# Optimization experiments

Measured on AMD Instinct MI355X. Metric: run time of the kernel, lower is better.

Reference implementation:

```python
import jax, jax.numpy as jnp
import numpy as np

B, S, HID = 2, 2048, 2048
H, KVH, D = 16, 4, 128
GROUPS = H // KVH  # 4


def apply_rotary(x, cos, sin):
    # x: [B, h, S, D]; cos/sin: [S, D//2]
    xr = x[..., 0::2]
    xi = x[..., 1::2]
    c = cos[None, None, :, :]
    s = sin[None, None, :, :]
    orr = xr * c - xi * s
    oi = xr * s + xi * c
    return jnp.stack([orr, oi], axis=-1).reshape(x.shape)


def setup_inputs() -> dict:
    key = jax.random.key(0)
    k0, k1, k2, k3, k4 = jax.random.split(key, 5)
    x = jax.random.normal(k0, (B, S, HID), dtype=jnp.float32)
    # real RoPE frequencies (llama-style), stored as [S, D//2, 2] = (cos, sin)
    inv_freq = 1.0 / (10000.0 ** (np.arange(0, D, 2, dtype=np.float32) / D))
    t = np.arange(S, dtype=np.float32)
    ang = np.outer(t, inv_freq)  # [S, D//2]
    freqs_cis = jnp.asarray(np.stack([np.cos(ang), np.sin(ang)], axis=-1), dtype=jnp.float32)
    sc = 0.02
    wq = jax.random.normal(k1, (HID, H * D), dtype=jnp.float32) * sc
    wk = jax.random.normal(k2, (HID, KVH * D), dtype=jnp.float32) * sc
    wv = jax.random.normal(k3, (HID, KVH * D), dtype=jnp.float32) * sc
    wo = jax.random.normal(k4, (H * D, HID), dtype=jnp.float32) * sc
    return {"x": x, "freqs_cis": freqs_cis, "wq": wq, "wk": wk, "wv": wv, "wo": wo}


def reference(x, freqs_cis, wq, wk, wv, wo):
    b, s, _ = x.shape
    cos, sin = freqs_cis[..., 0], freqs_cis[..., 1]
    q = (x @ wq).reshape(b, s, H, D).transpose(0, 2, 1, 3)    # [B,H,S,D]
    k = (x @ wk).reshape(b, s, KVH, D).transpose(0, 2, 1, 3)  # [B,KVH,S,D]
    v = (x @ wv).reshape(b, s, KVH, D).transpose(0, 2, 1, 3)
    q = apply_rotary(q, cos, sin)
    k = apply_rotary(k, cos, sin)
    # GQA expand: repeat kv heads into query-head groups
    k = jnp.repeat(k, GROUPS, axis=1)  # [B,H,S,D]
    v = jnp.repeat(v, GROUPS, axis=1)
    scale = 1.0 / jnp.sqrt(jnp.asarray(D, dtype=x.dtype))
    scores = jnp.einsum("bhqd,bhkd->bhqk", q, k) * scale
    causal = jnp.tril(jnp.ones((s, s), dtype=bool))
    scores = jnp.where(causal[None, None], scores, jnp.asarray(-jnp.inf, dtype=scores.dtype))
    attn = jax.nn.softmax(scores, axis=-1)
    out = jnp.einsum("bhqk,bhkd->bhqd", attn, v)
    out = out.transpose(0, 2, 1, 3).reshape(b, s, H * D)
    return out @ wo
```

## Files before the change

### kernel.cpp

```cpp
#include <hip/hip_runtime.h>
#include <hip/hip_bf16.h>

#define B_   2
#define S_   2048
#define HID_ 2048
#define H_   16
#define KVH_ 4
#define D_   128
#define M_   4096
#define NQKV 3072

typedef __attribute__((ext_vector_type(8))) short bf16x8;
typedef __attribute__((ext_vector_type(4))) float f32x4;
typedef const __attribute__((address_space(1))) unsigned int* gas_p;
typedef __attribute__((address_space(3))) unsigned int* las_p;

__device__ __forceinline__ unsigned short f2b(float f) {
    __hip_bfloat16 h = __float2bfloat16(f);
    return *reinterpret_cast<unsigned short*>(&h);
}
__device__ __forceinline__ float b2f(unsigned short u) {
    __hip_bfloat16 h;
    *reinterpret_cast<unsigned short*>(&h) = u;
    return __bfloat162float(h);
}

__global__ __launch_bounds__(256)
void convert_x(const float* __restrict__ x, unsigned short* __restrict__ xb) {
    int i = (blockIdx.x * 256 + threadIdx.x) * 4;
    float4 v = *(const float4*)(x + i);
    ushort4 o;
    o.x = f2b(v.x); o.y = f2b(v.y); o.z = f2b(v.z); o.w = f2b(v.w);
    *(ushort4*)(xb + i) = o;
}

__global__ __launch_bounds__(256)
void convert_w_t(const float* __restrict__ w, int N,
                 unsigned short* __restrict__ wt, int nbase) {
    __shared__ float tile[32][33];
    int tx = threadIdx.x & 31, ty = threadIdx.x >> 5;
    int n0 = blockIdx.x * 32, k0 = blockIdx.y * 32;
    #pragma unroll
    for (int j = 0; j < 4; j++)
        tile[ty + j*8][tx] = w[(size_t)(k0 + ty + j*8) * N + n0 + tx];
    __syncthreads();
    #pragma unroll
    for (int j = 0; j < 4; j++)
        wt[(size_t)(nbase + n0 + ty + j*8) * 2048 + k0 + tx] = f2b(tile[tx][ty + j*8]);
}

template<bool BF16OUT>
__global__ __launch_bounds__(256)
void gemm_bt(const unsigned short* __restrict__ A,
             const unsigned short* __restrict__ BT,
             void* __restrict__ Cv, int N) {
    __shared__ unsigned short As[128][32];
    __shared__ unsigned short Bs[128][32];

    int tid  = threadIdx.x;
    int lane = tid & 63, w = tid >> 6;
    int quad = lane >> 4, l15 = lane & 15;
    int row0 = blockIdx.y * 128, col0 = blockIdx.x * 128;
    int wm = (w & 1) * 64, wn = (w >> 1) * 64;

    f32x4 acc[4][4];
    const f32x4 zf = {0.f, 0.f, 0.f, 0.f};
    #pragma unroll
    for (int i = 0; i < 4; i++)
        #pragma unroll
        for (int j = 0; j < 4; j++) acc[i][j] = zf;

    const unsigned short* Arow = A  + (size_t)row0 * 2048;
    const unsigned short* Brow = BT + (size_t)col0 * 2048;

    for (int k0 = 0; k0 < 2048; k0 += 32) {
        #pragma unroll
        for (int it = 0; it < 2; it++) {
            int c = w * 128 + it * 64 + lane;
            int r = c >> 2, q8 = (c & 3) * 8;
            __builtin_amdgcn_global_load_lds(
                (gas_p)(Arow + (size_t)r * 2048 + k0 + q8),
                (las_p)((char*)&As[0][0] + (size_t)(w * 128 + it * 64) * 16),
                16, 0, 0);
            __builtin_amdgcn_global_load_lds(
                (gas_p)(Brow + (size_t)r * 2048 + k0 + q8),
                (las_p)((char*)&Bs[0][0] + (size_t)(w * 128 + it * 64) * 16),
                16, 0, 0);
        }
        __syncthreads();
        bf16x8 af[4], bf[4];
        #pragma unroll
        for (int i = 0; i < 4; i++) af[i] = *(const bf16x8*)&As[wm + i*16 + l15][quad * 8];
        #pragma unroll
        for (int j = 0; j < 4; j++) bf[j] = *(const bf16x8*)&Bs[wn + j*16 + l15][quad * 8];
        #pragma unroll
        for (int i = 0; i < 4; i++)
            #pragma unroll
            for (int j = 0; j < 4; j++)
                acc[i][j] = __builtin_amdgcn_mfma_f32_16x16x32_bf16(af[i], bf[j], acc[i][j], 0, 0, 0);
        __syncthreads();
    }

    #pragma unroll
    for (int i = 0; i < 4; i++)
        #pragma unroll
        for (int j = 0; j < 4; j++)
            #pragma unroll
            for (int r = 0; r < 4; r++) {
                size_t idx = (size_t)(row0 + wm + i*16 + quad*4 + r) * N + col0 + wn + j*16 + l15;
                if (BF16OUT) ((unsigned short*)Cv)[idx] = f2b(acc[i][j][r]);
                else         ((float*)Cv)[idx] = acc[i][j][r];
            }
}

__global__ __launch_bounds__(256)
void rope_kernel(unsigned short* __restrict__ qkv, const float* __restrict__ freqs) {
    int p = blockIdx.x * 256 + threadIdx.x;
    int m = p / 1280;
    int cp = p - m * 1280;
    int col = cp * 2;
    int s = m & (S_ - 1);
    int d = col & (D_ - 1);
    unsigned short* ptr = qkv + (size_t)m * NQKV + col;
    ushort2 uv = *(ushort2*)ptr;
    float xr = b2f(uv.x), xi = b2f(uv.y);
    float cs = freqs[s * 128 + d], sn = freqs[s * 128 + d + 1];
    ushort2 ov;
    ov.x = f2b(xr * cs - xi * sn);
    ov.y = f2b(xr * sn + xi * cs);
    *(ushort2*)ptr = ov;
}

__global__ __launch_bounds__(256)
void v_transpose(const unsigned short* __restrict__ qkv, unsigned short* __restrict__ vT) {
    __shared__ unsigned short tile[32][34];
    int tx = threadIdx.x & 31, ty = threadIdx.x >> 5;
    int s0 = blockIdx.x * 32;
    int c0 = blockIdx.y * 32;
    int b  = blockIdx.z;
    #pragma unroll
    for (int j = 0; j < 4; j++)
        tile[ty + j*8][tx] = qkv[(size_t)(b*2048 + s0 + ty + j*8) * NQKV + 2560 + c0 + tx];
    __syncthreads();
    #pragma unroll
    for (int j = 0; j < 4; j++)
        vT[(size_t)(b*512 + c0 + ty + j*8) * 2048 + s0 + tx] = tile[tx][ty + j*8];
}

__global__ __launch_bounds__(256)
void attn_mfma(const unsigned short* __restrict__ qkv,
               const unsigned short* __restrict__ vT,
               unsigned short* __restrict__ ao) {
    __shared__ unsigned short Ks[64 * 128];
    __shared__ unsigned short Vt[128 * 64];

    int tid  = threadIdx.x;
    int lane = tid & 63, w = tid >> 6;
    int quad = lane >> 4, l15 = lane & 15;
    int qt = 31 - blockIdx.x;
    int h = blockIdx.y, b = blockIdx.z;
    int hk = h >> 2;
    int q0 = qt * 64;
    const float scale = 0.08838834764831845f;

    bf16x8 aq[4];
    {
        const unsigned short* qrow = qkv + (size_t)(b*2048 + q0 + w*16 + l15) * NQKV + h*128;
        #pragma unroll
        for (int k4 = 0; k4 < 4; k4++)
            aq[k4] = *(const bf16x8*)(qrow + k4*32 + quad*8);
    }

    int koff[4][4];
    #pragma unroll
    for (int j = 0; j < 4; j++) {
        int row = ((j >> 1) * 32) + ((l15 >> 2) * 8) + ((j & 1) * 4) + (l15 & 3);
        #pragma unroll
        for (int k4 = 0; k4 < 4; k4++) {
            int slot = (k4 * 4 + quad) ^ (row & 15);
            koff[j][k4] = (row * 16 + slot) * 8;
        }
    }
    int voff[8][2];
    #pragma unroll
    for (int jn = 0; jn < 8; jn++) {
        int row = jn * 16 + l15;
        #pragma unroll
        for (int sh = 0; sh < 2; sh++) {
            int slot = (sh * 4 + quad) ^ (row & 7);
            voff[jn][sh] = (row * 8 + slot) * 8;
        }
    }

    const unsigned short* kb0 = qkv + (size_t)(b*2048) * NQKV + 2048 + hk*128;
    const unsigned short* vb0 = vT + (size_t)(b*512 + hk*128) * 2048;

    auto stage_k = [&](int kt) {
        #pragma unroll
        for (int it = 0; it < 4; it++) {
            int s = w * 256 + it * 64 + lane;
            int r = s >> 4, qp = s & 15;
            int q = qp ^ (r & 15);
            __builtin_amdgcn_global_load_lds(
                (gas_p)(kb0 + (size_t)(kt*64 + r) * NQKV + q * 8),
                (las_p)((char*)&Ks[0] + (w * 256 + it * 64) * 16),
                16, 0, 0);
        }
    };
    auto stage_v = [&](int kt) {
        #pragma unroll
        for (int it = 0; it < 4; it++) {
            int s = w * 256 + it * 64 + lane;
            int r = s >> 3, qp = s & 7;
            int q = qp ^ (r & 7);
            __builtin_amdgcn_global_load_lds(
                (gas_p)(vb0 + (size_t)r * 2048 + kt*64 + q * 8),
                (las_p)((char*)&Vt[0] + (w * 256 + it * 64) * 16),
                16, 0, 0);
        }
    };

    f32x4 o_acc[8];
    const f32x4 zf = {0.f, 0.f, 0.f, 0.f};
    #pragma unroll
    for (int jn = 0; jn < 8; jn++) o_acc[jn] = zf;
    float m_i = -1e30f, l_i = 0.f;
    const int qglob = q0 + w*16 + l15;

    stage_k(0);
    for (int kt = 0; kt <= qt; kt++) {
        __syncthreads();
        stage_v(kt);

        f32x4 s_acc[4];
        #pragma unroll
        for (int j = 0; j < 4; j++) {
            s_acc[j] = zf;
            #pragma unroll
            for (int k4 = 0; k4 < 4; k4++) {
                bf16x8 ak = *(const bf16x8*)&Ks[koff[j][k4]];
                s_acc[j] = __builtin_amdgcn_mfma_f32_16x16x32_bf16(ak, aq[k4], s_acc[j], 0, 0, 0);
            }
        }

        float sv[4][4];
        #pragma unroll
        for (int j = 0; j < 4; j++)
            #pragma unroll
            for (int r = 0; r < 4; r++)
                sv[j][r] = s_acc[j][r] * scale;
        if (kt == qt) {
            #pragma unroll
            for (int j = 0; j < 4; j++)
                #pragma unroll
                for (int r = 0; r < 4; r++) {
                    int sloc = ((j >> 1) * 32) + quad*8 + ((j & 1) * 4) + r;
                    if (kt*64 + sloc > qglob) sv[j][r] = -1e30f;
                }
        }

        float mx = sv[0][0];
        #pragma unroll
        for (int j = 0; j < 4; j++)
            #pragma unroll
            for (int r = 0; r < 4; r++) mx = fmaxf(mx, sv[j][r]);
        mx = fmaxf(mx, __shfl_xor(mx, 16));
        mx = fmaxf(mx, __shfl_xor(mx, 32));
        float mnew = fmaxf(m_i, mx);
        float alpha = __expf(m_i - mnew);
        float p[4][4], rs = 0.f;
        #pragma unroll
        for (int j = 0; j < 4; j++)
            #pragma unroll
            for (int r = 0; r < 4; r++) {
                p[j][r] = __expf(sv[j][r] - mnew);
                rs += p[j][r];
            }
        l_i = l_i * alpha + rs;
        m_i = mnew;
        #pragma unroll
        for (int jn = 0; jn < 8; jn++)
            #pragma unroll
            for (int r = 0; r < 4; r++) o_acc[jn][r] *= alpha;

        bf16x8 pp0, pp1;
        #pragma unroll
        for (int r = 0; r < 4; r++) {
            pp0[r]     = (short)f2b(p[0][r]);
            pp0[r + 4] = (short)f2b(p[1][r]);
            pp1[r]     = (short)f2b(p[2][r]);
            pp1[r + 4] = (short)f2b(p[3][r]);
        }

        __syncthreads();
        if (kt < qt) stage_k(kt + 1);

        #pragma unroll
        for (int jn = 0; jn < 8; jn++) {
            bf16x8 av0 = *(const bf16x8*)&Vt[voff[jn][0]];
            bf16x8 av1 = *(const bf16x8*)&Vt[voff[jn][1]];
            o_acc[jn] = __builtin_amdgcn_mfma_f32_16x16x32_bf16(av0, pp0, o_acc[jn], 0, 0, 0);
            o_acc[jn] = __builtin_amdgcn_mfma_f32_16x16x32_bf16(av1, pp1, o_acc[jn], 0, 0, 0);
        }
    }

    float lt = l_i;
    lt += __shfl_xor(lt, 16);
    lt += __shfl_xor(lt, 32);
    float inv = 1.f / lt;

    size_t base = (size_t)(b*2048 + qglob) * 2048 + h*128;
    #pragma unroll
    for (int jn = 0; jn < 8; jn++) {
        ushort4 ov;
        ov.x = f2b(o_acc[jn][0] * inv);
        ov.y = f2b(o_acc[jn][1] * inv);
        ov.z = f2b(o_acc[jn][2] * inv);
        ov.w = f2b(o_acc[jn][3] * inv);
        *(ushort4*)(ao + base + jn*16 + quad*4) = ov;
    }
}

extern "C" void kernel_launch(void* const* d_in, const int* in_sizes, int n_in,
                              void* d_out, int out_size, void* d_ws, size_t ws_size,
                              hipStream_t stream) {
    const float* x     = (const float*)d_in[0];
    const float* freqs = (const float*)d_in[1];
    const float* wq    = (const float*)d_in[2];
    const float* wk    = (const float*)d_in[3];
    const float* wv    = (const float*)d_in[4];
    const float* wo    = (const float*)d_in[5];
    float* out = (float*)d_out;

    char* ws = (char*)d_ws;
    unsigned short* xbf    = (unsigned short*)(ws);
    unsigned short* aobuf  = (unsigned short*)(ws);
    unsigned short* wqkvT  = (unsigned short*)(ws + (16u<<20));
    unsigned short* woT    = (unsigned short*)(ws + (28u<<20));
    unsigned short* qkvbuf = (unsigned short*)(ws + (36u<<20));
    unsigned short* vTbuf  = (unsigned short*)(ws + (60u<<20));

    dim3 blk(256);
    convert_x<<<8192, blk, 0, stream>>>(x, xbf);
    convert_w_t<<<dim3(64, 64), blk, 0, stream>>>(wq, 2048, wqkvT, 0);
    convert_w_t<<<dim3(16, 64), blk, 0, stream>>>(wk,  512, wqkvT, 2048);
    convert_w_t<<<dim3(16, 64), blk, 0, stream>>>(wv,  512, wqkvT, 2560);
    convert_w_t<<<dim3(64, 64), blk, 0, stream>>>(wo, 2048, woT, 0);

    gemm_bt<true><<<dim3(NQKV/128, M_/128), blk, 0, stream>>>(xbf, wqkvT, qkvbuf, NQKV);
    rope_kernel<<<20480, blk, 0, stream>>>(qkvbuf, freqs);
    v_transpose<<<dim3(64, 16, 2), blk, 0, stream>>>(qkvbuf, vTbuf);
    attn_mfma<<<dim3(32, 16, 2), blk, 0, stream>>>(qkvbuf, vTbuf, aobuf);
    gemm_bt<false><<<dim3(2048/128, M_/128), blk, 0, stream>>>(aobuf, woT, out, 2048);
}
```

Before: 355.8 us.

## Split long causal query tiles across two blocks and merge partial softmax results

The attention kernel now runs with 128 threads per block, and each wave handles two 16-row query fragments so that every K fragment read from LDS feeds two MFMAs. Query tiles in the upper half of the causal range have their KV loop split across two blocks. One half writes an unnormalised-merge partial output plus (max, sum) statistics into workspace, and a new merge kernel rescales and combines the two halves into the output. The aim is to balance the triangular causal workload and shorten the tail, at the cost of an extra launch, workspace traffic and a bf16 round-trip on the partial outputs.

```diff
diff --git a/kernel.cpp b/kernel.cpp
--- a/kernel.cpp
+++ b/kernel.cpp
@@ -147,28 +147,43 @@
         vT[(size_t)(b*512 + c0 + ty + j*8) * 2048 + s0 + tx] = tile[tx][ty + j*8];
 }
 
-__global__ __launch_bounds__(256)
+__global__ __launch_bounds__(128)
 void attn_mfma(const unsigned short* __restrict__ qkv,
                const unsigned short* __restrict__ vT,
-               unsigned short* __restrict__ ao) {
+               unsigned short* __restrict__ ao,
+               unsigned short* __restrict__ wsP,
+               float2* __restrict__ wsML) {
     __shared__ unsigned short Ks[64 * 128];
     __shared__ unsigned short Vt[128 * 64];
 
     int tid  = threadIdx.x;
     int lane = tid & 63, w = tid >> 6;
     int quad = lane >> 4, l15 = lane & 15;
-    int qt = 31 - blockIdx.x;
-    int h = blockIdx.y, b = blockIdx.z;
+    int bx = blockIdx.x, h = blockIdx.y, b = blockIdx.z;
     int hk = h >> 2;
+
+    int qt, c;
+    bool split = (bx < 32);
+    if (split) { qt = 31 - (bx >> 1); c = bx & 1; }
+    else       { qt = 47 - bx;        c = 0;      }
+    int nt = qt + 1;
+    int kt_begin = 0, kt_end = nt;
+    if (split) {
+        int nt0 = (nt + 1) >> 1;
+        kt_begin = c ? nt0 : 0;
+        kt_end   = c ? nt  : nt0;
+    }
     int q0 = qt * 64;
     const float scale = 0.08838834764831845f;
 
-    bf16x8 aq[4];
-    {
-        const unsigned short* qrow = qkv + (size_t)(b*2048 + q0 + w*16 + l15) * NQKV + h*128;
+    bf16x8 aq[2][4];
+    #pragma unroll
+    for (int qf = 0; qf < 2; qf++) {
+        const unsigned short* qrow =
+            qkv + (size_t)(b*2048 + q0 + w*32 + qf*16 + l15) * NQKV + h*128;
         #pragma unroll
         for (int k4 = 0; k4 < 4; k4++)
-            aq[k4] = *(const bf16x8*)(qrow + k4*32 + quad*8);
+            aq[qf][k4] = *(const bf16x8*)(qrow + k4*32 + quad*8);
     }
 
     int koff[4][4];
@@ -181,144 +196,190 @@
             koff[j][k4] = (row * 16 + slot) * 8;
         }
     }
-    int voff[8][2];
-    #pragma unroll
-    for (int jn = 0; jn < 8; jn++) {
-        int row = jn * 16 + l15;
-        #pragma unroll
-        for (int sh = 0; sh < 2; sh++) {
-            int slot = (sh * 4 + quad) ^ (row & 7);
-            voff[jn][sh] = (row * 8 + slot) * 8;
-        }
-    }
+    int vbase0 = (l15 * 8 + (quad ^ (l15 & 7))) * 8;
+    int vbase1 = (l15 * 8 + ((4 + quad) ^ (l15 & 7))) * 8;
 
     const unsigned short* kb0 = qkv + (size_t)(b*2048) * NQKV + 2048 + hk*128;
     const unsigned short* vb0 = vT + (size_t)(b*512 + hk*128) * 2048;
 
     auto stage_k = [&](int kt) {
         #pragma unroll
-        for (int it = 0; it < 4; it++) {
-            int s = w * 256 + it * 64 + lane;
+        for (int it = 0; it < 8; it++) {
+            int s = w * 512 + it * 64 + lane;
             int r = s >> 4, qp = s & 15;
             int q = qp ^ (r & 15);
             __builtin_amdgcn_global_load_lds(
                 (gas_p)(kb0 + (size_t)(kt*64 + r) * NQKV + q * 8),
-                (las_p)((char*)&Ks[0] + (w * 256 + it * 64) * 16),
+                (las_p)((char*)&Ks[0] + (w * 512 + it * 64) * 16),
                 16, 0, 0);
         }
     };
     auto stage_v = [&](int kt) {
         #pragma unroll
-        for (int it = 0; it < 4; it++) {
-            int s = w * 256 + it * 64 + lane;
+        for (int it = 0; it < 8; it++) {
+            int s = w * 512 + it * 64 + lane;
             int r = s >> 3, qp = s & 7;
             int q = qp ^ (r & 7);
             __builtin_amdgcn_global_load_lds(
                 (gas_p)(vb0 + (size_t)r * 2048 + kt*64 + q * 8),
-                (las_p)((char*)&Vt[0] + (w * 256 + it * 64) * 16),
+                (las_p)((char*)&Vt[0] + (w * 512 + it * 64) * 16),
                 16, 0, 0);
         }
     };
 
-    f32x4 o_acc[8];
+    f32x4 o_acc[2][8];
     const f32x4 zf = {0.f, 0.f, 0.f, 0.f};
     #pragma unroll
-    for (int jn = 0; jn < 8; jn++) o_acc[jn] = zf;
-    float m_i = -1e30f, l_i = 0.f;
-    const int qglob = q0 + w*16 + l15;
-
-    stage_k(0);
-    for (int kt = 0; kt <= qt; kt++) {
+    for (int qf = 0; qf < 2; qf++)
+        #pragma unroll
+        for (int jn = 0; jn < 8; jn++) o_acc[qf][jn] = zf;
+    float m_i[2] = {-1e30f, -1e30f}, l_i[2] = {0.f, 0.f};
+    int qglob[2] = {q0 + w*32 + l15, q0 + w*32 + 16 + l15};
+
+    stage_k(kt_begin);
+    for (int kt = kt_begin; kt < kt_end; kt++) {
         __syncthreads();
         stage_v(kt);
 
-        f32x4 s_acc[4];
+        f32x4 s_acc[2][4];
         #pragma unroll
         for (int j = 0; j < 4; j++) {
-            s_acc[j] = zf;
+            s_acc[0][j] = zf; s_acc[1][j] = zf;
             #pragma unroll
             for (int k4 = 0; k4 < 4; k4++) {
                 bf16x8 ak = *(const bf16x8*)&Ks[koff[j][k4]];
-                s_acc[j] = __builtin_amdgcn_mfma_f32_16x16x32_bf16(ak, aq[k4], s_acc[j], 0, 0, 0);
+                s_acc[0][j] = __builtin_amdgcn_mfma_f32_16x16x32_bf16(ak, aq[0][k4], s_acc[0][j], 0, 0, 0);
+                s_acc[1][j] = __builtin_amdgcn_mfma_f32_16x16x32_bf16(ak, aq[1][k4], s_acc[1][j], 0, 0, 0);
             }
         }
 
-        float sv[4][4];
-        #pragma unroll
-        for (int j = 0; j < 4; j++)
-            #pragma unroll
-            for (int r = 0; r < 4; r++)
-                sv[j][r] = s_acc[j][r] * scale;
-        if (kt == qt) {
+        bf16x8 pp[2][2];
+        #pragma unroll
+        for (int qf = 0; qf < 2; qf++) {
+            float sv[4][4];
+            #pragma unroll
+            for (int j = 0; j < 4; j++)
+                #pragma unroll
+                for (int r = 0; r < 4; r++)
+                    sv[j][r] = s_acc[qf][j][r] * scale;
+            if (kt == qt) {
+                #pragma unroll
+                for (int j = 0; j < 4; j++)
+                    #pragma unroll
+                    for (int r = 0; r < 4; r++) {
+                        int sloc = ((j >> 1) * 32) + quad*8 + ((j & 1) * 4) + r;
+                        if (kt*64 + sloc > qglob[qf]) sv[j][r] = -1e30f;
+                    }
+            }
+            float mx = sv[0][0];
+            #pragma unroll
+            for (int j = 0; j < 4; j++)
+                #pragma unroll
+                for (int r = 0; r < 4; r++) mx = fmaxf(mx, sv[j][r]);
+            mx = fmaxf(mx, __shfl_xor(mx, 16));
+            mx = fmaxf(mx, __shfl_xor(mx, 32));
+            float mnew = fmaxf(m_i[qf], mx);
+            float alpha = __expf(m_i[qf] - mnew);
+            float rs = 0.f;
+            float p[4][4];
             #pragma unroll
             for (int j = 0; j < 4; j++)
                 #pragma unroll
                 for (int r = 0; r < 4; r++) {
-                    int sloc = ((j >> 1) * 32) + quad*8 + ((j & 1) * 4) + r;
-                    if (kt*64 + sloc > qglob) sv[j][r] = -1e30f;
+                    p[j][r] = __expf(sv[j][r] - mnew);
+                    rs += p[j][r];
                 }
-        }
-
-        float mx = sv[0][0];
-        #pragma unroll
-        for (int j = 0; j < 4; j++)
-            #pragma unroll
-            for (int r = 0; r < 4; r++) mx = fmaxf(mx, sv[j][r]);
-        mx = fmaxf(mx, __shfl_xor(mx, 16));
-        mx = fmaxf(mx, __shfl_xor(mx, 32));
-        float mnew = fmaxf(m_i, mx);
-        float alpha = __expf(m_i - mnew);
-        float p[4][4], rs = 0.f;
-        #pragma unroll
-        for (int j = 0; j < 4; j++)
+            l_i[qf] = l_i[qf] * alpha + rs;
+            m_i[qf] = mnew;
+            #pragma unroll
+            for (int jn = 0; jn < 8; jn++)
+                #pragma unroll
+                for (int r = 0; r < 4; r++) o_acc[qf][jn][r] *= alpha;
             #pragma unroll
             for (int r = 0; r < 4; r++) {
-                p[j][r] = __expf(sv[j][r] - mnew);
-                rs += p[j][r];
+                pp[qf][0][r]     = (short)f2b(p[0][r]);
+                pp[qf][0][r + 4] = (short)f2b(p[1][r]);
+                pp[qf][1][r]     = (short)f2b(p[2][r]);
+                pp[qf][1][r + 4] = (short)f2b(p[3][r]);
             }
-        l_i = l_i * alpha + rs;
-        m_i = mnew;
-        #pragma unroll
-        for (int jn = 0; jn < 8; jn++)
-            #pragma unroll
-            for (int r = 0; r < 4; r++) o_acc[jn][r] *= alpha;
-
-        bf16x8 pp0, pp1;
-        #pragma unroll
-        for (int r = 0; r < 4; r++) {
-            pp0[r]     = (short)f2b(p[0][r]);
-            pp0[r + 4] = (short)f2b(p[1][r]);
-            pp1[r]     = (short)f2b(p[2][r]);
-            pp1[r + 4] = (short)f2b(p[3][r]);
         }
 
         __syncthreads();
-        if (kt < qt) stage_k(kt + 1);
+        if (kt + 1 < kt_end) stage_k(kt + 1);
 
         #pragma unroll
         for (int jn = 0; jn < 8; jn++) {
-            bf16x8 av0 = *(const bf16x8*)&Vt[voff[jn][0]];
-            bf16x8 av1 = *(const bf16x8*)&Vt[voff[jn][1]];
-            o_acc[jn] = __builtin_amdgcn_mfma_f32_16x16x32_bf16(av0, pp0, o_acc[jn], 0, 0, 0);
-            o_acc[jn] = __builtin_amdgcn_mfma_f32_16x16x32_bf16(av1, pp1, o_acc[jn], 0, 0, 0);
-        }
-    }
-
-    float lt = l_i;
-    lt += __shfl_xor(lt, 16);
-    lt += __shfl_xor(lt, 32);
-    float inv = 1.f / lt;
-
-    size_t base = (size_t)(b*2048 + qglob) * 2048 + h*128;
-    #pragma unroll
-    for (int jn = 0; jn < 8; jn++) {
-        ushort4 ov;
-        ov.x = f2b(o_acc[jn][0] * inv);
-        ov.y = f2b(o_acc[jn][1] * inv);
-        ov.z = f2b(o_acc[jn][2] * inv);
-        ov.w = f2b(o_acc[jn][3] * inv);
-        *(ushort4*)(ao + base + jn*16 + quad*4) = ov;
-    }
+            bf16x8 av0 = *(const bf16x8*)&Vt[jn*1024 + vbase0];
+            bf16x8 av1 = *(const bf16x8*)&Vt[jn*1024 + vbase1];
+            o_acc[0][jn] = __builtin_amdgcn_mfma_f32_16x16x32_bf16(av0, pp[0][0], o_acc[0][jn], 0, 0, 0);
+            o_acc[0][jn] = __builtin_amdgcn_mfma_f32_16x16x32_bf16(av1, pp[0][1], o_acc[0][jn], 0, 0, 0);
+            o_acc[1][jn] = __builtin_amdgcn_mfma_f32_16x16x32_bf16(av0, pp[1][0], o_acc[1][jn], 0, 0, 0);
+            o_acc[1][jn] = __builtin_amdgcn_mfma_f32_16x16x32_bf16(av1, pp[1][1], o_acc[1][jn], 0, 0, 0);
+        }
+    }
+
+    int pidx = ((qt - 16) * 16 + h) * 2 + b;
+    #pragma unroll
+    for (int qf = 0; qf < 2; qf++) {
+        float lt = l_i[qf];
+        lt += __shfl_xor(lt, 16);
+        lt += __shfl_xor(lt, 32);
+        float inv = 1.f / lt;
+        int q_local = w*32 + qf*16 + l15;
+        unsigned short* dst;
+        if (!split || c == 1)
+            dst = ao + (size_t)(b*2048 + q0 + q_local) * 2048 + h*128;
+        else
+            dst = wsP + (size_t)pidx * 8192 + q_local * 128;
+        #pragma unroll
+        for (int jn = 0; jn < 8; jn++) {
+            ushort4 ov;
+            ov.x = f2b(o_acc[qf][jn][0] * inv);
+            ov.y = f2b(o_acc[qf][jn][1] * inv);
+            ov.z = f2b(o_acc[qf][jn][2] * inv);
+            ov.w = f2b(o_acc[qf][jn][3] * inv);
+            *(ushort4*)(dst + jn*16 + quad*4) = ov;
+        }
+        if (split && quad == 0)
+            wsML[(pidx*2 + c) * 64 + q_local] = make_float2(m_i[qf], lt);
+    }
+}
+
+__global__ __launch_bounds__(256)
+void merge_kernel(unsigned short* __restrict__ ao,
+                  const unsigned short* __restrict__ wsP,
+                  const float2* __restrict__ wsML) {
+    int t = blockIdx.x * 256 + threadIdx.x;
+    int d  = (t & 15) * 8;
+    int h  = (t >> 4) & 15;
+    int qg = 1024 + ((t >> 8) & 1023);
+    int b  = t >> 18;
+    int qt = qg >> 6, q_local = qg & 63;
+    int pidx = ((qt - 16) * 16 + h) * 2 + b;
+
+    float2 ml0 = wsML[(pidx*2 + 0) * 64 + q_local];
+    float2 ml1 = wsML[(pidx*2 + 1) * 64 + q_local];
+    float mm = fmaxf(ml0.x, ml1.x);
+    float f0 = __expf(ml0.x - mm) * ml0.y;
+    float f1 = __expf(ml1.x - mm) * ml1.y;
+    float inv = 1.f / (f0 + f1);
+    f0 *= inv; f1 *= inv;
+
+    unsigned short* arow = ao + (size_t)(b*2048 + qg) * 2048 + h*128 + d;
+    const unsigned short* prow = wsP + (size_t)pidx * 8192 + q_local * 128 + d;
+    ushort4 a0 = *(ushort4*)arow,        a1 = *(ushort4*)(arow + 4);
+    ushort4 p0 = *(const ushort4*)prow,  p1 = *(const ushort4*)(prow + 4);
+    ushort4 o0, o1;
+    o0.x = f2b(f1*b2f(a0.x) + f0*b2f(p0.x));
+    o0.y = f2b(f1*b2f(a0.y) + f0*b2f(p0.y));
+    o0.z = f2b(f1*b2f(a0.z) + f0*b2f(p0.z));
+    o0.w = f2b(f1*b2f(a0.w) + f0*b2f(p0.w));
+    o1.x = f2b(f1*b2f(a1.x) + f0*b2f(p1.x));
+    o1.y = f2b(f1*b2f(a1.y) + f0*b2f(p1.y));
+    o1.z = f2b(f1*b2f(a1.z) + f0*b2f(p1.z));
+    o1.w = f2b(f1*b2f(a1.w) + f0*b2f(p1.w));
+    *(ushort4*)arow = o0;
+    *(ushort4*)(arow + 4) = o1;
 }
 
 extern "C" void kernel_launch(void* const* d_in, const int* in_sizes, int n_in,
@@ -339,6 +400,8 @@
     unsigned short* woT    = (unsigned short*)(ws + (28u<<20));
     unsigned short* qkvbuf = (unsigned short*)(ws + (36u<<20));
     unsigned short* vTbuf  = (unsigned short*)(ws + (60u<<20));
+    unsigned short* wsP    = (unsigned short*)(ws + (16u<<20));
+    float2*         wsML   = (float2*)(ws + (24u<<20));
 
     dim3 blk(256);
     convert_x<<<8192, blk, 0, stream>>>(x, xbf);
@@ -350,6 +413,7 @@
     gemm_bt<true><<<dim3(NQKV/128, M_/128), blk, 0, stream>>>(xbf, wqkvT, qkvbuf, NQKV);
     rope_kernel<<<20480, blk, 0, stream>>>(qkvbuf, freqs);
     v_transpose<<<dim3(64, 16, 2), blk, 0, stream>>>(qkvbuf, vTbuf);
-    attn_mfma<<<dim3(32, 16, 2), blk, 0, stream>>>(qkvbuf, vTbuf, aobuf);
+    attn_mfma<<<dim3(48, 16, 2), dim3(128), 0, stream>>>(qkvbuf, vTbuf, aobuf, wsP, wsML);
+    merge_kernel<<<2048, blk, 0, stream>>>(aobuf, wsP, wsML);
     gemm_bt<false><<<dim3(2048/128, M_/128), blk, 0, stream>>>(aobuf, woT, out, 2048);
 }
```

Result: no change. 353.8 us (-0.6%).
